# Kernel optimization log

Hardware: AMD Instinct MI355X
Metric: run time of the kernel (lower is better)

## Reference

```python
import jax, jax.numpy as jnp
import numpy as np

B, S = 16, 512
IN_DIM, ATTN_DIM, DEPTH, HEADS, DH = 512, 512, 4, 8, 64
CB_DIM, CB_SIZE, MAX_SEQ = 64, 8192, 544


def _ln(x, g, b):
    mu = x.mean(-1, keepdims=True)
    v = ((x - mu) ** 2).mean(-1, keepdims=True)
    return (x - mu) / jnp.sqrt(v + 1e-5) * g + b


def setup_inputs() -> dict:
    key = jax.random.key(0)
    ks = jax.random.split(key, 16)
    sc = 0.02
    d = {
        "x": jax.random.normal(ks[0], (B, S, IN_DIM), jnp.float32),
        "w_in": jax.random.normal(ks[1], (IN_DIM, ATTN_DIM), jnp.float32) * sc,
        "b_in": jnp.zeros((ATTN_DIM,), jnp.float32),
        "pos_emb": jax.random.normal(ks[2], (MAX_SEQ, ATTN_DIM), jnp.float32) * sc,
        "ln1_g": jnp.ones((DEPTH, ATTN_DIM), jnp.float32),
        "ln1_b": jnp.zeros((DEPTH, ATTN_DIM), jnp.float32),
        "wq": jax.random.normal(ks[3], (DEPTH, ATTN_DIM, ATTN_DIM), jnp.float32) * sc,
        "wk": jax.random.normal(ks[4], (DEPTH, ATTN_DIM, ATTN_DIM), jnp.float32) * sc,
        "wv": jax.random.normal(ks[5], (DEPTH, ATTN_DIM, ATTN_DIM), jnp.float32) * sc,
        "wo": jax.random.normal(ks[6], (DEPTH, ATTN_DIM, ATTN_DIM), jnp.float32) * sc,
        "ln2_g": jnp.ones((DEPTH, ATTN_DIM), jnp.float32),
        "ln2_b": jnp.zeros((DEPTH, ATTN_DIM), jnp.float32),
        "ff_w1": jax.random.normal(ks[7], (DEPTH, ATTN_DIM, 4 * ATTN_DIM), jnp.float32) * sc,
        "ff_b1": jnp.zeros((DEPTH, 4 * ATTN_DIM), jnp.float32),
        "ff_w2": jax.random.normal(ks[8], (DEPTH, 4 * ATTN_DIM, ATTN_DIM), jnp.float32) * sc,
        "ff_b2": jnp.zeros((DEPTH, ATTN_DIM), jnp.float32),
        "lnf_g": jnp.ones((ATTN_DIM,), jnp.float32),
        "lnf_b": jnp.zeros((ATTN_DIM,), jnp.float32),
        "w_out": jax.random.normal(ks[9], (ATTN_DIM, CB_DIM), jnp.float32) * sc,
        "b_out": jnp.zeros((CB_DIM,), jnp.float32),
        "codebook": jax.random.normal(ks[10], (CB_SIZE, CB_DIM), jnp.float32),
    }
    return d


def _attn(h, wq, wk, wv, wo):
    b, s, _ = h.shape
    q = jnp.einsum('bsd,de->bse', h, wq).reshape(b, s, HEADS, DH)
    k = jnp.einsum('bsd,de->bse', h, wk).reshape(b, s, HEADS, DH)
    v = jnp.einsum('bsd,de->bse', h, wv).reshape(b, s, HEADS, DH)
    scores = jnp.einsum('bqhd,bkhd->bhqk', q, k) * (DH ** -0.5)
    a = jax.nn.softmax(scores, axis=-1)
    o = jnp.einsum('bhqk,bkhd->bqhd', a, v).reshape(b, s, ATTN_DIM)
    return jnp.einsum('bse,ed->bsd', o, wo)


def reference(x, w_in, b_in, pos_emb, ln1_g, ln1_b, wq, wk, wv, wo,
              ln2_g, ln2_b, ff_w1, ff_b1, ff_w2, ff_b2, lnf_g, lnf_b,
              w_out, b_out, codebook):
    s = x.shape[1]
    # ContinuousTransformerWrapper: project in + absolute pos emb
    h = jnp.einsum('bsd,de->bse', x, w_in) + b_in + pos_emb[:s]
    # pre-norm encoder layers: attn + ff, each residual
    for i in range(DEPTH):
        h = h + _attn(_ln(h, ln1_g[i], ln1_b[i]), wq[i], wk[i], wv[i], wo[i])
        g = _ln(h, ln2_g[i], ln2_b[i])
        g = jax.nn.gelu(jnp.einsum('bsd,df->bsf', g, ff_w1[i]) + ff_b1[i])
        h = h + jnp.einsum('bsf,fd->bsd', g, ff_w2[i]) + ff_b2[i]
    h = _ln(h, lnf_g, lnf_b)
    z = jnp.einsum('bsd,dc->bsc', h, w_out) + b_out  # [B,S,CB_DIM]
    # VectorQuantize: euclidean nearest codebook entry
    d2 = (z ** 2).sum(-1, keepdims=True) - 2.0 * jnp.einsum('bsc,kc->bsk', z, codebook) \
         + (codebook ** 2).sum(-1)  # [B,S,CB_SIZE]
    idx = jnp.argmin(d2, axis=-1)
    q = codebook[idx]  # [B,S,CB_DIM]
    commit_loss = jnp.mean((jax.lax.stop_gradient(q) - z) ** 2)  # commitment_weight=1.0
    q_st = z + jax.lax.stop_gradient(q - z)  # straight-through
    return q_st.sum(axis=1), commit_loss
```

## Files before the change

kernel.cpp:

```cpp
#include <hip/hip_runtime.h>
#include <cmath>

#define BATCH 16
#define SEQ 512
#define DMODEL 512
#define NDEPTH 4
#define NHEADS 8
#define DHEAD 64
#define DFF 2048
#define CBD 64
#define CBS 8192
#define MROWS (BATCH * SEQ)

typedef unsigned short u16;
typedef __attribute__((ext_vector_type(8))) short short8;
typedef __attribute__((ext_vector_type(4))) float f32x4;
typedef __attribute__((ext_vector_type(4))) unsigned short u16x4;

__device__ __forceinline__ u16 f2bf(float f) {
    unsigned u = __float_as_uint(f);
    u += 0x7fff + ((u >> 16) & 1);
    return (u16)(u >> 16);
}
__device__ __forceinline__ float bf2f(u16 h) {
    return __uint_as_float(((unsigned)h) << 16);
}

__device__ __forceinline__ void async16(u16* lds, const u16* g) {
    __builtin_amdgcn_global_load_lds(
        (const __attribute__((address_space(1))) unsigned int*)g,
        (__attribute__((address_space(3))) unsigned int*)lds, 16, 0, 0);
}

__device__ __forceinline__ float gelu_tanh(float u) {
    float t = fmaf(0.07135481627f * u, u * u, 1.5957691216f * u);
    return u / (1.0f + __expf(-t));
}

__global__ void zero_kernel(float* __restrict__ p, int n) {
    int i = blockIdx.x * 256 + threadIdx.x;
    if (i < n) p[i] = 0.0f;
}

__global__ void cbn_kernel(const float* __restrict__ cb, float* __restrict__ cbn) {
    int c = blockIdx.x * 256 + threadIdx.x;
    if (c >= CBS) return;
    const float* row = cb + (size_t)c * CBD;
    float s = 0.0f;
#pragma unroll
    for (int d = 0; d < CBD; ++d) s += row[d] * row[d];
    cbn[c] = s;
}

__global__ __launch_bounds__(256) void wtrans_kernel(
    const float* __restrict__ W, u16* __restrict__ Th, u16* __restrict__ Tl,
    int K, int N, long inLS, long outLS) {
    __shared__ float t[32][33];
    const float* Ws = W + (size_t)blockIdx.z * inLS;
    u16* Tho = Th + (size_t)blockIdx.z * outLS;
    u16* Tlo = Tl + (size_t)blockIdx.z * outLS;
    int n0 = blockIdx.x * 32, k0 = blockIdx.y * 32;
    int tx = threadIdx.x & 31, ty = threadIdx.x >> 5;
#pragma unroll
    for (int r = ty; r < 32; r += 8) t[r][tx] = Ws[(size_t)(k0 + r) * N + n0 + tx];
    __syncthreads();
#pragma unroll
    for (int r = ty; r < 32; r += 8) {
        float v = t[tx][r];
        size_t o = (size_t)(n0 + r) * K + k0 + tx;
        u16 hh = f2bf(v);
        Tho[o] = hh;
        Tlo[o] = f2bf(v - bf2f(hh));
    }
}

__global__ __launch_bounds__(256) void vtrans_kernel(
    const u16* __restrict__ Qh, const u16* __restrict__ Ql,
    u16* __restrict__ VTh, u16* __restrict__ VTl) {
    __shared__ u16 t[64][68];
    int s0 = blockIdx.x * 64;
    int hh = blockIdx.y;
    int b = blockIdx.z & 15, plane = blockIdx.z >> 4;
    const u16* src = (plane ? Ql : Qh) + ((size_t)(16 + hh) * MROWS) * 64;
    u16* dst = (plane ? VTl : VTh);
    int tid = threadIdx.x;
    int rr = tid >> 4, c4 = (tid & 15) * 4;
#pragma unroll
    for (int i = 0; i < 4; ++i) {
        int r = rr + i * 16;
        const u16* p = src + (size_t)(b * SEQ + s0 + r) * 64 + c4;
        *(u16x4*)(&t[r][c4]) = *(const u16x4*)p;
    }
    __syncthreads();
#pragma unroll
    for (int i = 0; i < 4; ++i) {
        int r = rr + i * 16;
        u16x4 v;
        v.x = t[c4 + 0][r]; v.y = t[c4 + 1][r]; v.z = t[c4 + 2][r]; v.w = t[c4 + 3][r];
        *(u16x4*)(dst + (size_t)b * SEQ * DMODEL + (size_t)(hh * 64 + r) * SEQ + s0 + c4) = v;
    }
}

__global__ void split_kernel(const float* __restrict__ X, u16* __restrict__ H,
                             u16* __restrict__ L, int n) {
    int i = blockIdx.x * 256 + threadIdx.x;
    if (i < n) {
        float v = X[i];
        u16 hh = f2bf(v);
        H[i] = hh;
        L[i] = f2bf(v - bf2f(hh));
    }
}

__global__ __launch_bounds__(256) void ln_kernel(
    const float* __restrict__ X,
    const float* __restrict__ C0, const float* __restrict__ C1,
    const float* __restrict__ bias2, const float* __restrict__ pos2,
    float* __restrict__ Xout,
    float* __restrict__ Y, u16* __restrict__ Yh, u16* __restrict__ Yl,
    const float* __restrict__ g, const float* __restrict__ b) {
    int row  = blockIdx.x * 4 + (threadIdx.x >> 6);
    int lane = threadIdx.x & 63;
    float v[8];
    float s = 0.0f;
#pragma unroll
    for (int j = 0; j < 8; ++j) {
        int d = lane + j * 64;
        size_t o = (size_t)row * DMODEL + d;
        float t = X ? X[o] : 0.0f;
        if (C0)    t += C0[o] + C1[o];
        if (bias2) t += bias2[d];
        if (pos2)  t += pos2[(size_t)(row & (SEQ - 1)) * DMODEL + d];
        v[j] = t;
        if (Xout) Xout[o] = t;
        s += t;
    }
#pragma unroll
    for (int off = 32; off; off >>= 1) s += __shfl_xor(s, off);
    float mu  = s * (1.0f / DMODEL);
    float var = 0.0f;
#pragma unroll
    for (int j = 0; j < 8; ++j) { float d = v[j] - mu; var += d * d; }
#pragma unroll
    for (int off = 32; off; off >>= 1) var += __shfl_xor(var, off);
    float r = rsqrtf(var * (1.0f / DMODEL) + 1e-5f);
#pragma unroll
    for (int j = 0; j < 8; ++j) {
        int d = lane + j * 64;
        float y = (v[j] - mu) * r * g[d] + b[d];
        size_t o = (size_t)row * DMODEL + d;
        if (Y) Y[o] = y;
        if (Yh) {
            u16 hh = f2bf(y);
            Yh[o] = hh;
            Yl[o] = f2bf(y - bf2f(hh));
        }
    }
}

__global__ __launch_bounds__(256) void gemm3_kernel(
    const u16* __restrict__ Ah, const u16* __restrict__ Al,
    const u16* __restrict__ Bh, const u16* __restrict__ Bl,
    float* __restrict__ Cf, u16* __restrict__ Ch, u16* __restrict__ Cl,
    const float* __restrict__ bias, const float* __restrict__ res,
    const float* __restrict__ pos, int M, int N, int K, int gelu,
    float* __restrict__ Cs0, float* __restrict__ Cs1, int kslice, int qkvscatter) {
    __shared__ __align__(16) u16 AsH[128 * 64];
    __shared__ __align__(16) u16 AsL[128 * 64];
    __shared__ __align__(16) u16 BsH[128 * 64];
    __shared__ __align__(16) u16 BsL[128 * 64];

    int tid  = threadIdx.x;
    int w    = tid >> 6, lane = tid & 63;
    int wr   = w >> 1, wc = w & 1;
    int quad = lane >> 4, l16 = lane & 15;
    int m0   = blockIdx.x * 128;
    int n0   = blockIdx.y * 128;
    int ksA  = (kslice > 0) ? blockIdx.z * kslice : 0;
    int ksB  = (kslice > 0) ? ksA + kslice : K;

    f32x4 acc[4][4];
#pragma unroll
    for (int i = 0; i < 4; ++i)
#pragma unroll
        for (int j = 0; j < 4; ++j) acc[i][j] = (f32x4){0.f, 0.f, 0.f, 0.f};

    int ldsoff[4];
    size_t goff[4];
#pragma unroll
    for (int r = 0; r < 4; ++r) {
        int cidx = tid + 256 * r;
        int row = cidx >> 3;
        int cg = (cidx & 7) ^ (row & 7);
        ldsoff[r] = cidx * 8;
        goff[r] = (size_t)row * K + cg * 8;
    }

    const u16* AbaseH = Ah + (size_t)m0 * K;
    const u16* AbaseL = Al + (size_t)m0 * K;
    const u16* BbaseH = Bh + (size_t)n0 * K;
    const u16* BbaseL = Bl + (size_t)n0 * K;

    for (int ks = ksA; ks < ksB; ks += 64) {
        __syncthreads();
#pragma unroll
        for (int r = 0; r < 4; ++r) {
            size_t g = goff[r] + ks;
            async16(&AsH[ldsoff[r]], AbaseH + g);
            async16(&AsL[ldsoff[r]], AbaseL + g);
            async16(&BsH[ldsoff[r]], BbaseH + g);
            async16(&BsL[ldsoff[r]], BbaseL + g);
        }
        __syncthreads();
#pragma unroll
        for (int s = 0; s < 2; ++s) {
            short8 afh[4], afl[4];
#pragma unroll
            for (int i = 0; i < 4; ++i) {
                int row = wr * 64 + i * 16 + l16;
                int off = row * 64 + (((s << 2) | quad) ^ (row & 7)) * 8;
                afh[i] = *(const short8*)&AsH[off];
                afl[i] = *(const short8*)&AsL[off];
            }
#pragma unroll
            for (int j = 0; j < 4; ++j) {
                int rowb = wc * 64 + j * 16 + l16;
                int offb = rowb * 64 + (((s << 2) | quad) ^ (rowb & 7)) * 8;
                short8 bh = *(const short8*)&BsH[offb];
                short8 bl = *(const short8*)&BsL[offb];
#pragma unroll
                for (int i = 0; i < 4; ++i) {
                    acc[i][j] = __builtin_amdgcn_mfma_f32_16x16x32_bf16(afh[i], bh, acc[i][j], 0, 0, 0);
                    acc[i][j] = __builtin_amdgcn_mfma_f32_16x16x32_bf16(afl[i], bh, acc[i][j], 0, 0, 0);
                    acc[i][j] = __builtin_amdgcn_mfma_f32_16x16x32_bf16(afh[i], bl, acc[i][j], 0, 0, 0);
                }
            }
        }
    }

    float* Cspl = (kslice > 0) ? (blockIdx.z ? Cs1 : Cs0) : nullptr;
    int mbase = m0 + wr * 64;
    int nbase = n0 + wc * 64;
#pragma unroll
    for (int mi = 0; mi < 4; ++mi)
#pragma unroll
        for (int ni = 0; ni < 4; ++ni) {
            f32x4 a = acc[mi][ni];
#pragma unroll
            for (int r = 0; r < 4; ++r) {
                int m = mbase + mi * 16 + quad * 4 + r;
                int n = nbase + ni * 16 + l16;
                float v = a[r];
                size_t o = qkvscatter
                    ? ((size_t)(n >> 6) * M + m) * 64 + (n & 63)
                    : (size_t)m * N + n;
                if (Cspl) { Cspl[o] = v; continue; }
                if (bias) v += bias[n];
                if (pos)  v += pos[(size_t)(m & (SEQ - 1)) * N + n];
                if (res)  v += res[(size_t)m * N + n];
                if (gelu) v = gelu_tanh(v);
                if (Cf) Cf[o] = v;
                if (Ch) {
                    u16 hh = f2bf(v);
                    Ch[o] = hh;
                    Cl[o] = f2bf(v - bf2f(hh));
                }
            }
        }
}

__global__ __launch_bounds__(256) void gemm_kernel(
    const float* __restrict__ A, const float* __restrict__ Bm,
    float* __restrict__ C, const float* __restrict__ bias,
    int M, int N, int K) {
    __shared__ float As[16][68];
    __shared__ float Bs[16][64];
    int tid = threadIdx.x;
    int tx = tid & 15, ty = tid >> 4;
    int a_m = tid >> 2, a_k = (tid & 3) * 4;
    int b_k = tid >> 4, b_n = (tid & 15) * 4;
    const float* Arow = A + (size_t)(blockIdx.x * 64 + a_m) * K;
    const float* Bcol = Bm + (size_t)blockIdx.y * 64 + b_n;
    float acc[4][4] = {};
    for (int k0 = 0; k0 < K; k0 += 16) {
        float4 av = *(const float4*)(Arow + k0 + a_k);
        float4 bv = *(const float4*)(Bcol + (size_t)(k0 + b_k) * N);
        __syncthreads();
        As[a_k + 0][a_m] = av.x; As[a_k + 1][a_m] = av.y;
        As[a_k + 2][a_m] = av.z; As[a_k + 3][a_m] = av.w;
        *(float4*)(&Bs[b_k][b_n]) = bv;
        __syncthreads();
#pragma unroll
        for (int kk = 0; kk < 16; ++kk) {
            float4 a4 = *(const float4*)(&As[kk][ty * 4]);
            float4 b4 = *(const float4*)(&Bs[kk][tx * 4]);
            float ar[4] = {a4.x, a4.y, a4.z, a4.w};
            float br[4] = {b4.x, b4.y, b4.z, b4.w};
#pragma unroll
            for (int i = 0; i < 4; ++i)
#pragma unroll
                for (int j = 0; j < 4; ++j) acc[i][j] = fmaf(ar[i], br[j], acc[i][j]);
        }
    }
    int m0 = blockIdx.x * 64 + ty * 4;
    int n0 = blockIdx.y * 64 + tx * 4;
#pragma unroll
    for (int i = 0; i < 4; ++i) {
        float vv[4];
#pragma unroll
        for (int j = 0; j < 4; ++j) {
            float t = acc[i][j];
            if (bias) t += bias[n0 + j];
            vv[j] = t;
        }
        *(float4*)(C + (size_t)(m0 + i) * N + n0) = make_float4(vv[0], vv[1], vv[2], vv[3]);
    }
}

__global__ __launch_bounds__(256) void attn_flash_kernel(
    const u16* __restrict__ QKh, const u16* __restrict__ QKl,
    const u16* __restrict__ VTh, const u16* __restrict__ VTl,
    u16* __restrict__ Oh, u16* __restrict__ Ol) {
    int bh = blockIdx.x & 127;
    int qt = blockIdx.x >> 7;
    int bb = bh >> 3, hh = bh & 7;

    __shared__ __align__(16) float Pw[4][16 * 68];

    int tid = threadIdx.x;
    int w = tid >> 6, lane = tid & 63;
    int quad = lane >> 4, l16 = lane & 15;
    int qtile = qt * 4 + w;
    float* P = Pw[w];

    const u16* qrh = QKh + ((size_t)hh * MROWS + bb * SEQ + qtile * 16 + l16) * 64 + quad * 8;
    const u16* qrl = QKl + ((size_t)hh * MROWS + bb * SEQ + qtile * 16 + l16) * 64 + quad * 8;
    short8 Qh0 = *(const short8*)qrh;
    short8 Qh1 = *(const short8*)(qrh + 32);
    short8 Ql0 = *(const short8*)qrl;
    short8 Ql1 = *(const short8*)(qrl + 32);

    float lsum[4] = {0.f, 0.f, 0.f, 0.f};
    f32x4 acc[4];
#pragma unroll
    for (int dt = 0; dt < 4; ++dt) acc[dt] = (f32x4){0.f, 0.f, 0.f, 0.f};

    const u16* KbH = QKh + ((size_t)(8 + hh) * MROWS + bb * SEQ) * 64;
    const u16* KbL = QKl + ((size_t)(8 + hh) * MROWS + bb * SEQ) * 64;
    const u16* VbH = VTh + (size_t)bb * SEQ * DMODEL + (size_t)(hh * 64) * SEQ;
    const u16* VbL = VTl + (size_t)bb * SEQ * DMODEL + (size_t)(hh * 64) * SEQ;

    for (int kt = 0; kt < 8; ++kt) {
        int kb = kt * 64;
#pragma unroll
        for (int s = 0; s < 4; ++s) {
            const u16* kh = KbH + (size_t)(kb + s * 16 + l16) * 64 + quad * 8;
            const u16* kl = KbL + (size_t)(kb + s * 16 + l16) * 64 + quad * 8;
            f32x4 a = (f32x4){0.f, 0.f, 0.f, 0.f};
            {
                short8 Kh0 = *(const short8*)kh;
                short8 Kh1 = *(const short8*)(kh + 32);
                a = __builtin_amdgcn_mfma_f32_16x16x32_bf16(Qh0, Kh0, a, 0, 0, 0);
                a = __builtin_amdgcn_mfma_f32_16x16x32_bf16(Qh1, Kh1, a, 0, 0, 0);
                a = __builtin_amdgcn_mfma_f32_16x16x32_bf16(Ql0, Kh0, a, 0, 0, 0);
                a = __builtin_amdgcn_mfma_f32_16x16x32_bf16(Ql1, Kh1, a, 0, 0, 0);
            }
            {
                short8 Kl0 = *(const short8*)kl;
                short8 Kl1 = *(const short8*)(kl + 32);
                a = __builtin_amdgcn_mfma_f32_16x16x32_bf16(Qh0, Kl0, a, 0, 0, 0);
                a = __builtin_amdgcn_mfma_f32_16x16x32_bf16(Qh1, Kl1, a, 0, 0, 0);
            }
#pragma unroll
            for (int r = 0; r < 4; ++r) {
                float p = __expf(a[r] * 0.125f);
                lsum[r] += p;
                P[(quad * 4 + r) * 68 + s * 16 + l16] = p;
            }
        }
#pragma unroll
        for (int ks = 0; ks < 2; ++ks) {
            short8 ph, pl;
            {
                const float* src = &P[l16 * 68 + ks * 32 + quad * 8];
                f32x4 a0 = *(const f32x4*)src;
                f32x4 a1 = *(const f32x4*)(src + 4);
                float v[8] = {a0[0], a0[1], a0[2], a0[3], a1[0], a1[1], a1[2], a1[3]};
#pragma unroll
                for (int j = 0; j < 8; ++j) {
                    u16 hv = f2bf(v[j]);
                    ph[j] = (short)hv;
                    pl[j] = (short)f2bf(v[j] - bf2f(hv));
                }
            }
#pragma unroll
            for (int dt = 0; dt < 4; ++dt) {
                const u16* vh = VbH + (size_t)(dt * 16 + l16) * SEQ + kb + ks * 32 + quad * 8;
                const u16* vl = VbL + (size_t)(dt * 16 + l16) * SEQ + kb + ks * 32 + quad * 8;
                short8 Vh = *(const short8*)vh;
                short8 Vl = *(const short8*)vl;
                acc[dt] = __builtin_amdgcn_mfma_f32_16x16x32_bf16(ph, Vh, acc[dt], 0, 0, 0);
                acc[dt] = __builtin_amdgcn_mfma_f32_16x16x32_bf16(pl, Vh, acc[dt], 0, 0, 0);
                acc[dt] = __builtin_amdgcn_mfma_f32_16x16x32_bf16(ph, Vl, acc[dt], 0, 0, 0);
            }
        }
    }

#pragma unroll
    for (int r = 0; r < 4; ++r) {
#pragma unroll
        for (int off = 8; off; off >>= 1) lsum[r] += __shfl_xor(lsum[r], off);
    }
#pragma unroll
    for (int r = 0; r < 4; ++r) {
        float inv = 1.0f / lsum[r];
        size_t rowoff = (size_t)(bb * SEQ + qtile * 16 + quad * 4 + r) * DMODEL + hh * 64;
#pragma unroll
        for (int dt = 0; dt < 4; ++dt) {
            float v = acc[dt][r] * inv;
            u16 hv = f2bf(v);
            Oh[rowoff + dt * 16 + l16] = hv;
            Ol[rowoff + dt * 16 + l16] = f2bf(v - bf2f(hv));
        }
    }
}

__global__ __launch_bounds__(256) void vq3_kernel(
    const float* __restrict__ Z, const u16* __restrict__ Zh, const u16* __restrict__ Zl,
    const u16* __restrict__ CBh, const u16* __restrict__ CBl,
    const float* __restrict__ CB, const float* __restrict__ CBN,
    float* __restrict__ out) {
    __shared__ float sbest[4][16];
    __shared__ int sidx[4][16];
    __shared__ int ibest[16];
    __shared__ float psum[4][64];
    __shared__ float cl4[4];

    int tid = threadIdx.x;
    int w = tid >> 6, lane = tid & 63;
    int quad = lane >> 4, l16 = lane & 15;
    int row0 = blockIdx.x * 16;

    const u16* zph = Zh + (size_t)(row0 + l16) * CBD + quad * 8;
    const u16* zpl = Zl + (size_t)(row0 + l16) * CBD + quad * 8;
    short8 Z0h = *(const short8*)zph;
    short8 Z1h = *(const short8*)(zph + 32);
    short8 Z0l = *(const short8*)zpl;
    short8 Z1l = *(const short8*)(zpl + 32);

    float best[4] = {3.4e38f, 3.4e38f, 3.4e38f, 3.4e38f};
    int bidx[4] = {0, 0, 0, 0};

    int cbase = w * (CBS / 4);
#pragma unroll 2
    for (int t = 0; t < CBS / 4; t += 16) {
        int code = cbase + t + l16;
        const u16* cph = CBh + (size_t)code * CBD + quad * 8;
        const u16* cpl = CBl + (size_t)code * CBD + quad * 8;
        short8 C0h = *(const short8*)cph;
        short8 C1h = *(const short8*)(cph + 32);
        short8 C0l = *(const short8*)cpl;
        short8 C1l = *(const short8*)(cpl + 32);
        float cn = CBN[code];
        f32x4 a = (f32x4){0.f, 0.f, 0.f, 0.f};
        a = __builtin_amdgcn_mfma_f32_16x16x32_bf16(Z0h, C0h, a, 0, 0, 0);
        a = __builtin_amdgcn_mfma_f32_16x16x32_bf16(Z1h, C1h, a, 0, 0, 0);
        a = __builtin_amdgcn_mfma_f32_16x16x32_bf16(Z0l, C0h, a, 0, 0, 0);
        a = __builtin_amdgcn_mfma_f32_16x16x32_bf16(Z1l, C1h, a, 0, 0, 0);
        a = __builtin_amdgcn_mfma_f32_16x16x32_bf16(Z0h, C0l, a, 0, 0, 0);
        a = __builtin_amdgcn_mfma_f32_16x16x32_bf16(Z1h, C1l, a, 0, 0, 0);
#pragma unroll
        for (int r = 0; r < 4; ++r) {
            float s = cn - 2.0f * a[r];
            if (s < best[r]) { best[r] = s; bidx[r] = code; }
        }
    }
#pragma unroll
    for (int off = 8; off; off >>= 1) {
#pragma unroll
        for (int r = 0; r < 4; ++r) {
            float ov = __shfl_xor(best[r], off);
            int oi = __shfl_xor(bidx[r], off);
            if (ov < best[r] || (ov == best[r] && oi < bidx[r])) { best[r] = ov; bidx[r] = oi; }
        }
    }
    if (l16 == 0) {
#pragma unroll
        for (int r = 0; r < 4; ++r) {
            sbest[w][quad * 4 + r] = best[r];
            sidx[w][quad * 4 + r] = bidx[r];
        }
    }
    __syncthreads();
    if (tid < 16) {
        float bv = sbest[0][tid];
        int bi = sidx[0][tid];
#pragma unroll
        for (int ww = 1; ww < 4; ++ww) {
            float ov = sbest[ww][tid];
            int oi = sidx[ww][tid];
            if (ov < bv || (ov == bv && oi < bi)) { bv = ov; bi = oi; }
        }
        ibest[tid] = bi;
    }
    __syncthreads();

    int d2 = lane;
    float qacc = 0.0f, closs = 0.0f;
#pragma unroll
    for (int j = 0; j < 4; ++j) {
        int r2 = w * 4 + j;
        int bi = ibest[r2];
        float q = CB[(size_t)bi * CBD + d2];
        float z = Z[(size_t)(row0 + r2) * CBD + d2];
        qacc += q;
        float df = q - z;
        closs += df * df;
    }
    psum[w][d2] = qacc;
#pragma unroll
    for (int off = 32; off; off >>= 1) closs += __shfl_xor(closs, off);
    if (d2 == 0) cl4[w] = closs;
    __syncthreads();
    if (tid < 64) {
        float t = psum[0][tid] + psum[1][tid] + psum[2][tid] + psum[3][tid];
        int b = row0 >> 9;
        atomicAdd(out + b * 64 + tid, t);
    }
    if (tid == 0)
        atomicAdd(out + 1024, (cl4[0] + cl4[1] + cl4[2] + cl4[3]) * (1.0f / (float)(MROWS * CBD)));
}

extern "C" void kernel_launch(void* const* d_in, const int* in_sizes, int n_in,
                              void* d_out, int out_size, void* d_ws, size_t ws_size,
                              hipStream_t stream) {
    const float* x    = (const float*)d_in[0];
    const float* w_in = (const float*)d_in[1];
    const float* b_in = (const float*)d_in[2];
    const float* pos  = (const float*)d_in[3];
    const float* ln1g = (const float*)d_in[4];
    const float* ln1b = (const float*)d_in[5];
    const float* wq   = (const float*)d_in[6];
    const float* wk   = (const float*)d_in[7];
    const float* wv   = (const float*)d_in[8];
    const float* wo   = (const float*)d_in[9];
    const float* ln2g = (const float*)d_in[10];
    const float* ln2b = (const float*)d_in[11];
    const float* ffw1 = (const float*)d_in[12];
    const float* ffb1 = (const float*)d_in[13];
    const float* ffw2 = (const float*)d_in[14];
    const float* ffb2 = (const float*)d_in[15];
    const float* lnfg = (const float*)d_in[16];
    const float* lnfb = (const float*)d_in[17];
    const float* wout = (const float*)d_in[18];
    const float* bout = (const float*)d_in[19];
    const float* cb   = (const float*)d_in[20];
    float* out = (float*)d_out;

    const size_t MD  = (size_t)MROWS * DMODEL;
    const size_t MQ  = (size_t)MROWS * 1536;
    const size_t MF  = (size_t)MROWS * DFF;

    float* ws   = (float*)d_ws;
    float* h    = ws;
    float* t0   = h + MD;
    float* big  = t0 + MD;
    float* zb   = big + MF;
    float* cbn  = zb + (size_t)MROWS * CBD;
    u16* cbh    = (u16*)(cbn + CBS);
    u16* cbl    = cbh + (size_t)CBS * CBD;
    u16* t0h    = (u16*)(cbh + 2 * (size_t)CBS * CBD);
    u16* t0l    = t0h + MD;
    u16* wb     = t0l + MD;

    u16* qkvh = (u16*)big;
    u16* qkvl = qkvh + MQ;
    u16* obh  = qkvl + MQ;
    u16* obl  = obh + MD;
    u16* xh   = obh;
    u16* xl   = obl;
    u16* fmh  = (u16*)big;
    u16* fml  = fmh + MF;
    u16* zbh  = (u16*)big;
    u16* zbl  = zbh + (size_t)MROWS * CBD;

    const size_t S_WIN  = (size_t)DMODEL * DMODEL;
    const size_t S_QKV  = (size_t)1536 * DMODEL * NDEPTH;
    const size_t S_WO   = S_WIN * NDEPTH;
    const size_t S_FF1  = (size_t)DFF * DMODEL * NDEPTH;
    const size_t S_FF2  = S_FF1;
    u16* winT_h = wb;
    u16* winT_l = winT_h + S_WIN;
    u16* qkvT_h = winT_l + S_WIN;
    u16* qkvT_l = qkvT_h + S_QKV;
    u16* woT_h  = qkvT_l + S_QKV;
    u16* woT_l  = woT_h + S_WO;
    u16* ff1T_h = woT_l + S_WO;
    u16* ff1T_l = ff1T_h + S_FF1;
    u16* ff2T_h = ff1T_l + S_FF1;
    u16* ff2T_l = ff2T_h + S_FF2;
    u16* VTh = ff2T_l + S_FF2;
    u16* VTl = VTh + (size_t)BATCH * SEQ * DMODEL;
    float* spK0 = (float*)(VTl + (size_t)BATCH * SEQ * DMODEL);
    float* spK1 = spK0 + MD;

    dim3 blk(256);

    zero_kernel<<<dim3((out_size + 255) / 256), blk, 0, stream>>>(out, out_size);
    cbn_kernel<<<dim3(CBS / 256), blk, 0, stream>>>(cb, cbn);
    split_kernel<<<dim3((int)(CBS * CBD / 256)), blk, 0, stream>>>(cb, cbh, cbl, CBS * CBD);

    wtrans_kernel<<<dim3(16, 16, 1), blk, 0, stream>>>(w_in, winT_h, winT_l, DMODEL, DMODEL, 0, 0);
    wtrans_kernel<<<dim3(16, 16, NDEPTH), blk, 0, stream>>>(
        wq, qkvT_h, qkvT_l, DMODEL, DMODEL, (long)DMODEL * DMODEL, (long)1536 * DMODEL);
    wtrans_kernel<<<dim3(16, 16, NDEPTH), blk, 0, stream>>>(
        wk, qkvT_h + (size_t)512 * DMODEL, qkvT_l + (size_t)512 * DMODEL,
        DMODEL, DMODEL, (long)DMODEL * DMODEL, (long)1536 * DMODEL);
    wtrans_kernel<<<dim3(16, 16, NDEPTH), blk, 0, stream>>>(
        wv, qkvT_h + (size_t)1024 * DMODEL, qkvT_l + (size_t)1024 * DMODEL,
        DMODEL, DMODEL, (long)DMODEL * DMODEL, (long)1536 * DMODEL);
    wtrans_kernel<<<dim3(16, 16, NDEPTH), blk, 0, stream>>>(
        wo, woT_h, woT_l, DMODEL, DMODEL, (long)DMODEL * DMODEL, (long)DMODEL * DMODEL);
    wtrans_kernel<<<dim3(DFF / 32, 16, NDEPTH), blk, 0, stream>>>(
        ffw1, ff1T_h, ff1T_l, DMODEL, DFF, (long)DMODEL * DFF, (long)DFF * DMODEL);
    wtrans_kernel<<<dim3(16, DFF / 32, NDEPTH), blk, 0, stream>>>(
        ffw2, ff2T_h, ff2T_l, DFF, DMODEL, (long)DFF * DMODEL, (long)DMODEL * DFF);

    split_kernel<<<dim3((int)(MD / 256)), blk, 0, stream>>>(x, xh, xl, (int)MD);

    gemm3_kernel<<<dim3(MROWS / 128, DMODEL / 128, 2), blk, 0, stream>>>(
        xh, xl, winT_h, winT_l, nullptr, nullptr, nullptr, nullptr, nullptr, nullptr,
        MROWS, DMODEL, DMODEL, 0, spK0, spK1, 256, 0);

    for (int l = 0; l < NDEPTH; ++l) {
        ln_kernel<<<dim3(MROWS / 4), blk, 0, stream>>>(
            (l == 0) ? nullptr : h, spK0, spK1,
            (l == 0) ? b_in : (ffb2 + (size_t)(l - 1) * DMODEL),
            (l == 0) ? pos : nullptr, h,
            nullptr, t0h, t0l, ln1g + l * DMODEL, ln1b + l * DMODEL);
        gemm3_kernel<<<dim3(MROWS / 128, 1536 / 128, 1), blk, 0, stream>>>(
            t0h, t0l, qkvT_h + (size_t)l * 1536 * DMODEL, qkvT_l + (size_t)l * 1536 * DMODEL,
            nullptr, qkvh, qkvl, nullptr, nullptr, nullptr, MROWS, 1536, DMODEL, 0,
            nullptr, nullptr, 0, 1);
        vtrans_kernel<<<dim3(8, 8, 32), blk, 0, stream>>>(qkvh, qkvl, VTh, VTl);
        attn_flash_kernel<<<dim3(1024), blk, 0, stream>>>(
            qkvh, qkvl, VTh, VTl, obh, obl);
        gemm3_kernel<<<dim3(MROWS / 128, DMODEL / 128, 2), blk, 0, stream>>>(
            obh, obl, woT_h + (size_t)l * S_WIN, woT_l + (size_t)l * S_WIN,
            nullptr, nullptr, nullptr, nullptr, nullptr, nullptr,
            MROWS, DMODEL, DMODEL, 0, spK0, spK1, 256, 0);
        ln_kernel<<<dim3(MROWS / 4), blk, 0, stream>>>(
            h, spK0, spK1, nullptr, nullptr, h,
            nullptr, t0h, t0l, ln2g + l * DMODEL, ln2b + l * DMODEL);
        gemm3_kernel<<<dim3(MROWS / 128, DFF / 128, 1), blk, 0, stream>>>(
            t0h, t0l, ff1T_h + (size_t)l * DFF * DMODEL, ff1T_l + (size_t)l * DFF * DMODEL,
            nullptr, fmh, fml, ffb1 + l * DFF, nullptr, nullptr, MROWS, DFF, DMODEL, 1,
            nullptr, nullptr, 0, 0);
        gemm3_kernel<<<dim3(MROWS / 128, DMODEL / 128, 2), blk, 0, stream>>>(
            fmh, fml, ff2T_h + (size_t)l * DFF * DMODEL, ff2T_l + (size_t)l * DFF * DMODEL,
            nullptr, nullptr, nullptr, nullptr, nullptr, nullptr,
            MROWS, DMODEL, DFF, 0, spK0, spK1, 1024, 0);
    }

    ln_kernel<<<dim3(MROWS / 4), blk, 0, stream>>>(
        h, spK0, spK1, ffb2 + (size_t)3 * DMODEL, nullptr, nullptr,
        t0, nullptr, nullptr, lnfg, lnfb);
    gemm_kernel<<<dim3(MROWS / 64, 1), blk, 0, stream>>>(t0, wout, zb, bout, MROWS, CBD, DMODEL);
    split_kernel<<<dim3((int)((size_t)MROWS * CBD / 256)), blk, 0, stream>>>(
        zb, zbh, zbl, MROWS * CBD);
    vq3_kernel<<<dim3(MROWS / 16), blk, 0, stream>>>(zb, zbh, zbl, cbh, cbl, cb, cbn, out);
}
```

Baseline: 1.768 ms.

## Software-pipeline K/V loads in attention and codebook loads in VQ argmin

Restructures the attention inner loop to prefetch the next K tiles and V fragments into registers ahead of the MFMA work that consumes them, double-buffering K across key tiles. The VQ nearest-code search is rewritten with four rotating register buffers, so codebook loads for upcoming tiles are issued while the current tile is computed. The aim is to hide global-memory latency behind matrix instructions. The cost is higher register pressure, which may reduce occupancy, plus some redundant wraparound loads on the final iteration.

After: 1.876 ms. +6.1%, slower.

```diff
diff --git a/kernel.cpp b/kernel.cpp
--- a/kernel.cpp
+++ b/kernel.cpp
@@ -350,61 +350,96 @@
     const u16* VbH = VTh + (size_t)bb * SEQ * DMODEL + (size_t)(hh * 64) * SEQ;
     const u16* VbL = VTl + (size_t)bb * SEQ * DMODEL + (size_t)(hh * 64) * SEQ;
 
+    short8 Kah0, Kah1, Kal0, Kal1;
+    short8 Kbh0, Kbh1, Kbl0, Kbl1;
+    short8 V0h, V0l, V1h, V1l, V2h, V2l, V3h, V3l;
+    short8 ph, pl;
+
+#define LOADK(bk, row_) {                                          \
+    const u16* kh_ = KbH + (size_t)(row_) * 64 + quad * 8;         \
+    const u16* kl_ = KbL + (size_t)(row_) * 64 + quad * 8;         \
+    bk##h0 = *(const short8*)kh_;  bk##h1 = *(const short8*)(kh_ + 32); \
+    bk##l0 = *(const short8*)kl_;  bk##l1 = *(const short8*)(kl_ + 32); }
+
+#define QKC(bk, sidx_) {                                                        \
+    f32x4 a_ = (f32x4){0.f, 0.f, 0.f, 0.f};                                     \
+    a_ = __builtin_amdgcn_mfma_f32_16x16x32_bf16(Qh0, bk##h0, a_, 0, 0, 0);     \
+    a_ = __builtin_amdgcn_mfma_f32_16x16x32_bf16(Qh1, bk##h1, a_, 0, 0, 0);     \
+    a_ = __builtin_amdgcn_mfma_f32_16x16x32_bf16(Ql0, bk##h0, a_, 0, 0, 0);     \
+    a_ = __builtin_amdgcn_mfma_f32_16x16x32_bf16(Ql1, bk##h1, a_, 0, 0, 0);     \
+    a_ = __builtin_amdgcn_mfma_f32_16x16x32_bf16(Qh0, bk##l0, a_, 0, 0, 0);     \
+    a_ = __builtin_amdgcn_mfma_f32_16x16x32_bf16(Qh1, bk##l1, a_, 0, 0, 0);     \
+    _Pragma("unroll")                                                           \
+    for (int r = 0; r < 4; ++r) {                                               \
+        float p_ = __expf(a_[r] * 0.125f);                                      \
+        lsum[r] += p_;                                                          \
+        P[(quad * 4 + r) * 68 + (sidx_) * 16 + l16] = p_;                       \
+    } }
+
+#define LOADV(ks_) {                                                            \
+    size_t vcol_ = (size_t)kb + (ks_) * 32 + quad * 8;                          \
+    V0h = *(const short8*)(VbH + (size_t)(0 * 16 + l16) * SEQ + vcol_);         \
+    V0l = *(const short8*)(VbL + (size_t)(0 * 16 + l16) * SEQ + vcol_);         \
+    V1h = *(const short8*)(VbH + (size_t)(1 * 16 + l16) * SEQ + vcol_);         \
+    V1l = *(const short8*)(VbL + (size_t)(1 * 16 + l16) * SEQ + vcol_);         \
+    V2h = *(const short8*)(VbH + (size_t)(2 * 16 + l16) * SEQ + vcol_);         \
+    V2l = *(const short8*)(VbL + (size_t)(2 * 16 + l16) * SEQ + vcol_);         \
+    V3h = *(const short8*)(VbH + (size_t)(3 * 16 + l16) * SEQ + vcol_);         \
+    V3l = *(const short8*)(VbL + (size_t)(3 * 16 + l16) * SEQ + vcol_); }
+
+#define PACKP(ks_) {                                                            \
+    const float* src_ = &P[l16 * 68 + (ks_) * 32 + quad * 8];                   \
+    f32x4 a0_ = *(const f32x4*)src_;                                            \
+    f32x4 a1_ = *(const f32x4*)(src_ + 4);                                      \
+    float vv_[8] = {a0_[0], a0_[1], a0_[2], a0_[3], a1_[0], a1_[1], a1_[2], a1_[3]}; \
+    _Pragma("unroll")                                                           \
+    for (int j = 0; j < 8; ++j) {                                               \
+        u16 hv_ = f2bf(vv_[j]);                                                 \
+        ph[j] = (short)hv_;                                                     \
+        pl[j] = (short)f2bf(vv_[j] - bf2f(hv_));                                \
+    } }
+
+#define PVC() {                                                                 \
+    acc[0] = __builtin_amdgcn_mfma_f32_16x16x32_bf16(ph, V0h, acc[0], 0, 0, 0); \
+    acc[1] = __builtin_amdgcn_mfma_f32_16x16x32_bf16(ph, V1h, acc[1], 0, 0, 0); \
+    acc[2] = __builtin_amdgcn_mfma_f32_16x16x32_bf16(ph, V2h, acc[2], 0, 0, 0); \
+    acc[3] = __builtin_amdgcn_mfma_f32_16x16x32_bf16(ph, V3h, acc[3], 0, 0, 0); \
+    acc[0] = __builtin_amdgcn_mfma_f32_16x16x32_bf16(pl, V0h, acc[0], 0, 0, 0); \
+    acc[1] = __builtin_amdgcn_mfma_f32_16x16x32_bf16(pl, V1h, acc[1], 0, 0, 0); \
+    acc[2] = __builtin_amdgcn_mfma_f32_16x16x32_bf16(pl, V2h, acc[2], 0, 0, 0); \
+    acc[3] = __builtin_amdgcn_mfma_f32_16x16x32_bf16(pl, V3h, acc[3], 0, 0, 0); \
+    acc[0] = __builtin_amdgcn_mfma_f32_16x16x32_bf16(ph, V0l, acc[0], 0, 0, 0); \
+    acc[1] = __builtin_amdgcn_mfma_f32_16x16x32_bf16(ph, V1l, acc[1], 0, 0, 0); \
+    acc[2] = __builtin_amdgcn_mfma_f32_16x16x32_bf16(ph, V2l, acc[2], 0, 0, 0); \
+    acc[3] = __builtin_amdgcn_mfma_f32_16x16x32_bf16(ph, V3l, acc[3], 0, 0, 0); }
+
+    LOADK(Ka, 0 + l16);
+    LOADK(Kb, 16 + l16);
+
     for (int kt = 0; kt < 8; ++kt) {
-        int kb = kt * 64;
-#pragma unroll
-        for (int s = 0; s < 4; ++s) {
-            const u16* kh = KbH + (size_t)(kb + s * 16 + l16) * 64 + quad * 8;
-            const u16* kl = KbL + (size_t)(kb + s * 16 + l16) * 64 + quad * 8;
-            f32x4 a = (f32x4){0.f, 0.f, 0.f, 0.f};
-            {
-                short8 Kh0 = *(const short8*)kh;
-                short8 Kh1 = *(const short8*)(kh + 32);
-                a = __builtin_amdgcn_mfma_f32_16x16x32_bf16(Qh0, Kh0, a, 0, 0, 0);
-                a = __builtin_amdgcn_mfma_f32_16x16x32_bf16(Qh1, Kh1, a, 0, 0, 0);
-                a = __builtin_amdgcn_mfma_f32_16x16x32_bf16(Ql0, Kh0, a, 0, 0, 0);
-                a = __builtin_amdgcn_mfma_f32_16x16x32_bf16(Ql1, Kh1, a, 0, 0, 0);
-            }
-            {
-                short8 Kl0 = *(const short8*)kl;
-                short8 Kl1 = *(const short8*)(kl + 32);
-                a = __builtin_amdgcn_mfma_f32_16x16x32_bf16(Qh0, Kl0, a, 0, 0, 0);
-                a = __builtin_amdgcn_mfma_f32_16x16x32_bf16(Qh1, Kl1, a, 0, 0, 0);
-            }
-#pragma unroll
-            for (int r = 0; r < 4; ++r) {
-                float p = __expf(a[r] * 0.125f);
-                lsum[r] += p;
-                P[(quad * 4 + r) * 68 + s * 16 + l16] = p;
-            }
-        }
-#pragma unroll
-        for (int ks = 0; ks < 2; ++ks) {
-            short8 ph, pl;
-            {
-                const float* src = &P[l16 * 68 + ks * 32 + quad * 8];
-                f32x4 a0 = *(const f32x4*)src;
-                f32x4 a1 = *(const f32x4*)(src + 4);
-                float v[8] = {a0[0], a0[1], a0[2], a0[3], a1[0], a1[1], a1[2], a1[3]};
-#pragma unroll
-                for (int j = 0; j < 8; ++j) {
-                    u16 hv = f2bf(v[j]);
-                    ph[j] = (short)hv;
-                    pl[j] = (short)f2bf(v[j] - bf2f(hv));
-                }
-            }
-#pragma unroll
-            for (int dt = 0; dt < 4; ++dt) {
-                const u16* vh = VbH + (size_t)(dt * 16 + l16) * SEQ + kb + ks * 32 + quad * 8;
-                const u16* vl = VbL + (size_t)(dt * 16 + l16) * SEQ + kb + ks * 32 + quad * 8;
-                short8 Vh = *(const short8*)vh;
-                short8 Vl = *(const short8*)vl;
-                acc[dt] = __builtin_amdgcn_mfma_f32_16x16x32_bf16(ph, Vh, acc[dt], 0, 0, 0);
-                acc[dt] = __builtin_amdgcn_mfma_f32_16x16x32_bf16(pl, Vh, acc[dt], 0, 0, 0);
-                acc[dt] = __builtin_amdgcn_mfma_f32_16x16x32_bf16(ph, Vl, acc[dt], 0, 0, 0);
-            }
-        }
-    }
+        int kb  = kt * 64;
+        int kbn = ((kt + 1) & 7) * 64;
+        QKC(Ka, 0);
+        LOADK(Ka, kb + 32 + l16);
+        QKC(Kb, 1);
+        LOADK(Kb, kb + 48 + l16);
+        LOADV(0);
+        QKC(Ka, 2);
+        QKC(Kb, 3);
+        LOADK(Ka, kbn + 0 + l16);
+        LOADK(Kb, kbn + 16 + l16);
+        PACKP(0);
+        PVC();
+        LOADV(1);
+        PACKP(1);
+        PVC();
+    }
+
+#undef LOADK
+#undef QKC
+#undef LOADV
+#undef PACKP
+#undef PVC
 
 #pragma unroll
     for (int r = 0; r < 4; ++r) {
@@ -451,30 +486,50 @@
     float best[4] = {3.4e38f, 3.4e38f, 3.4e38f, 3.4e38f};
     int bidx[4] = {0, 0, 0, 0};
 
-    int cbase = w * (CBS / 4);
-#pragma unroll 2
-    for (int t = 0; t < CBS / 4; t += 16) {
-        int code = cbase + t + l16;
-        const u16* cph = CBh + (size_t)code * CBD + quad * 8;
-        const u16* cpl = CBl + (size_t)code * CBD + quad * 8;
-        short8 C0h = *(const short8*)cph;
-        short8 C1h = *(const short8*)(cph + 32);
-        short8 C0l = *(const short8*)cpl;
-        short8 C1l = *(const short8*)(cpl + 32);
-        float cn = CBN[code];
-        f32x4 a = (f32x4){0.f, 0.f, 0.f, 0.f};
-        a = __builtin_amdgcn_mfma_f32_16x16x32_bf16(Z0h, C0h, a, 0, 0, 0);
-        a = __builtin_amdgcn_mfma_f32_16x16x32_bf16(Z1h, C1h, a, 0, 0, 0);
-        a = __builtin_amdgcn_mfma_f32_16x16x32_bf16(Z0l, C0h, a, 0, 0, 0);
-        a = __builtin_amdgcn_mfma_f32_16x16x32_bf16(Z1l, C1h, a, 0, 0, 0);
-        a = __builtin_amdgcn_mfma_f32_16x16x32_bf16(Z0h, C0l, a, 0, 0, 0);
-        a = __builtin_amdgcn_mfma_f32_16x16x32_bf16(Z1h, C1l, a, 0, 0, 0);
-#pragma unroll
-        for (int r = 0; r < 4; ++r) {
-            float s = cn - 2.0f * a[r];
-            if (s < best[r]) { best[r] = s; bidx[r] = code; }
-        }
-    }
+    short8 A0h, A1h, A0l, A1l;  float An;
+    short8 B0h, B1h, B0l, B1l;  float Bn;
+    short8 C0h, C1h, C0l, C1l;  float Cn;
+    short8 D0h, D1h, D0l, D1l;  float Dn;
+
+#define LOADB(bk, cc) {                                            \
+    int c_ = (cc);                                                 \
+    const u16* ph_ = CBh + (size_t)c_ * CBD + quad * 8;            \
+    const u16* pl_ = CBl + (size_t)c_ * CBD + quad * 8;            \
+    bk##0h = *(const short8*)ph_;  bk##1h = *(const short8*)(ph_ + 32); \
+    bk##0l = *(const short8*)pl_;  bk##1l = *(const short8*)(pl_ + 32); \
+    bk##n  = CBN[c_]; }
+
+#define COMPB(bk, cc) {                                                          \
+    f32x4 a_ = (f32x4){0.f, 0.f, 0.f, 0.f};                                      \
+    int c_ = (cc);                                                               \
+    a_ = __builtin_amdgcn_mfma_f32_16x16x32_bf16(Z0h, bk##0h, a_, 0, 0, 0);      \
+    a_ = __builtin_amdgcn_mfma_f32_16x16x32_bf16(Z1h, bk##1h, a_, 0, 0, 0);      \
+    a_ = __builtin_amdgcn_mfma_f32_16x16x32_bf16(Z0l, bk##0h, a_, 0, 0, 0);      \
+    a_ = __builtin_amdgcn_mfma_f32_16x16x32_bf16(Z1l, bk##1h, a_, 0, 0, 0);      \
+    a_ = __builtin_amdgcn_mfma_f32_16x16x32_bf16(Z0h, bk##0l, a_, 0, 0, 0);      \
+    a_ = __builtin_amdgcn_mfma_f32_16x16x32_bf16(Z1h, bk##1l, a_, 0, 0, 0);      \
+    _Pragma("unroll")                                                            \
+    for (int r = 0; r < 4; ++r) {                                                \
+        float s_ = bk##n - 2.0f * a_[r];                                         \
+        if (s_ < best[r]) { best[r] = s_; bidx[r] = c_; }                        \
+    } }
+
+    const int NW = CBS / 4;
+    int cbase = w * NW;
+    LOADB(A, cbase + l16);
+    LOADB(B, cbase + 16 + l16);
+    LOADB(C, cbase + 32 + l16);
+    LOADB(D, cbase + 48 + l16);
+    for (int t = 0; t < NW; t += 64) {
+        COMPB(A, cbase + t + l16);       LOADB(A, cbase + ((t + 64)  & (NW - 1)) + l16);
+        COMPB(B, cbase + t + 16 + l16);  LOADB(B, cbase + ((t + 80)  & (NW - 1)) + l16);
+        COMPB(C, cbase + t + 32 + l16);  LOADB(C, cbase + ((t + 96)  & (NW - 1)) + l16);
+        COMPB(D, cbase + t + 48 + l16);  LOADB(D, cbase + ((t + 112) & (NW - 1)) + l16);
+    }
+
+#undef LOADB
+#undef COMPB
+
 #pragma unroll
     for (int off = 8; off; off >>= 1) {
 #pragma unroll
```
